# Optimization experiments

Hardware: AMD Instinct MI355X
Metric: run time of the kernel (lower is better)

Reference implementation:

```python
import jax, jax.numpy as jnp
import numpy as np
from jax import lax

B, T, C = 2, 2048, 2048
H, KV = 16, 4
D = C // H          # 128 head_dim
EPS = 1e-5
THETA = 10000.0
NEG = -1e9


def setup_inputs() -> dict:
    key = jax.random.key(0)
    ks = jax.random.split(key, 12)
    x = jax.random.normal(ks[0], (B, T, C), dtype=jnp.float32)
    s_in = 1.0 / np.sqrt(C)
    s_attn = 1.0 / np.sqrt(C)
    Wq = jax.random.normal(ks[1], (C, H * D), jnp.float32) * s_in
    Wk = jax.random.normal(ks[2], (C, KV * D), jnp.float32) * s_in
    Wv = jax.random.normal(ks[3], (C, KV * D), jnp.float32) * s_in
    Wo = jax.random.normal(ks[4], (H * D, C), jnp.float32) * s_attn
    bq = jnp.zeros((H * D,), jnp.float32)
    bk = jnp.zeros((KV * D,), jnp.float32)
    bv = jnp.zeros((KV * D,), jnp.float32)
    bo = jnp.zeros((C,), jnp.float32)
    qn_w = jnp.ones((D,), jnp.float32)
    kn_w = jnp.ones((D,), jnp.float32)
    # rotary tables: freqs_cis[t, j] = exp(i * t * theta^(-2j/D))
    inv_freq = 1.0 / (THETA ** (jnp.arange(0, D, 2, dtype=jnp.float32) / D))  # [D/2]
    angles = jnp.arange(T, dtype=jnp.float32)[:, None] * inv_freq[None, :]    # [T, D/2]
    freqs_cos = jnp.cos(angles)
    freqs_sin = jnp.sin(angles)
    # additive causal mask [1,1,T,T]
    causal = jnp.tril(jnp.ones((T, T), dtype=bool))
    mask = jnp.where(causal, 0.0, NEG).astype(jnp.float32)[None, None]
    return {"x": x, "Wq": Wq, "bq": bq, "Wk": Wk, "bk": bk, "Wv": Wv, "bv": bv,
            "Wo": Wo, "bo": bo, "qn_w": qn_w, "kn_w": kn_w,
            "freqs_cos": freqs_cos, "freqs_sin": freqs_sin, "mask": mask}


def _rmsnorm(h, w):
    var = jnp.mean(jnp.square(h), axis=-1, keepdims=True)
    return h * jax.lax.rsqrt(var + EPS) * w


def _rope(h, cos, sin):
    # h: [B,T,n,D]; cos/sin: [T, D/2] -> broadcast [1,T,1,D/2]
    hr = h.reshape(*h.shape[:-1], D // 2, 2)
    a, b = hr[..., 0], hr[..., 1]
    c = cos[None, :, None, :]
    s = sin[None, :, None, :]
    out = jnp.stack([a * c - b * s, a * s + b * c], axis=-1)
    return out.reshape(h.shape)


def reference(x, Wq, bq, Wk, bk, Wv, bv, Wo, bo, qn_w, kn_w, freqs_cos, freqs_sin, mask):
    q = (x @ Wq + bq).reshape(B, T, H, D)
    k = (x @ Wk + bk).reshape(B, T, KV, D)
    v = (x @ Wv + bv).reshape(B, T, KV, D)
    q = _rmsnorm(q, qn_w)
    k = _rmsnorm(k, kn_w)
    q = _rope(q, freqs_cos, freqs_sin)
    k = _rope(k, freqs_cos, freqs_sin)
    # GQA: repeat kv heads (interleaved, matching jnp.repeat on axis=2)
    k = jnp.repeat(k, H // KV, axis=2)
    v = jnp.repeat(v, H // KV, axis=2)
    q, k, v = (jnp.swapaxes(t, 1, 2) for t in (q, k, v))  # [B,H,T,D]
    scale = 1.0 / jnp.sqrt(jnp.float32(D))
    scores = jnp.einsum('bhid,bhjd->bhij', q, k) * scale + mask
    scores = scores - lax.stop_gradient(jnp.max(scores, axis=-1, keepdims=True))
    w = jnp.exp(scores)
    w = w / jnp.sum(w, axis=-1, keepdims=True)
    out = jnp.einsum('bhij,bhjd->bhid', w, v)
    out = jnp.swapaxes(out, 1, 2).reshape(B, T, H * D)
    return out @ Wo + bo
```

## Files before the change

kernel.cpp:

```cpp
#include <hip/hip_runtime.h>

typedef __bf16 bf16_t;
typedef __bf16 bf16x8 __attribute__((ext_vector_type(8)));
typedef __bf16 bf16x4 __attribute__((ext_vector_type(4)));
typedef float f32x4 __attribute__((ext_vector_type(4)));
typedef unsigned int u32;

#define B_    2
#define T_    2048
#define C_    2048
#define H_    16
#define KV_   4
#define D_    128
#define NT_   4096
#define NQKV_ 3072

__device__ __forceinline__ void gload16(const void* g, void* l) {
  __builtin_amdgcn_global_load_lds((const __attribute__((address_space(1))) u32*)g,
                                   (__attribute__((address_space(3))) u32*)l, 16, 0, 0);
}

__global__ __launch_bounds__(256) void k_convert(const float* __restrict__ x,
                                                 bf16_t* __restrict__ y, int n4) {
  int i = blockIdx.x * 256 + threadIdx.x;
  if (i >= n4) return;
  float4 v = ((const float4*)x)[i];
  bf16x4 o;
  o[0] = (bf16_t)v.x; o[1] = (bf16_t)v.y; o[2] = (bf16_t)v.z; o[3] = (bf16_t)v.w;
  ((bf16x4*)y)[i] = o;
}

__global__ __launch_bounds__(256) void k_transpose(const float* __restrict__ W,
                                                   bf16_t* __restrict__ Wt, int K, int N) {
  __shared__ float tile[32][33];
  int n0 = blockIdx.x * 32, k0 = blockIdx.y * 32;
  int tx = threadIdx.x & 31, ty = threadIdx.x >> 5;
#pragma unroll
  for (int r = 0; r < 32; r += 8)
    tile[ty + r][tx] = W[(size_t)(k0 + ty + r) * N + n0 + tx];
  __syncthreads();
#pragma unroll
  for (int r = 0; r < 32; r += 8)
    Wt[(size_t)(n0 + ty + r) * K + k0 + tx] = (bf16_t)tile[tx][ty + r];
}

__global__ void k_bias(const float* __restrict__ bq, const float* __restrict__ bk,
                       const float* __restrict__ bv, float* __restrict__ o) {
  int i = blockIdx.x * 256 + threadIdx.x;
  if (i < 2048) o[i] = bq[i];
  else if (i < 2560) o[i] = bk[i - 2048];
  else if (i < 3072) o[i] = bv[i - 2560];
}

__global__ __launch_bounds__(256) void k_gemm(const bf16_t* __restrict__ A,
                                              const bf16_t* __restrict__ Wt,
                                              const float* __restrict__ bias,
                                              float* __restrict__ Cout, int NTOT) {
  constexpr int K = 2048;
  __shared__ __align__(16) bf16_t As[2][128 * 32];
  __shared__ __align__(16) bf16_t Bs[2][128 * 32];
  const int tid = threadIdx.x;
  const int lane = tid & 63, w = tid >> 6;
  const int c = lane & 15, g = lane >> 4;
  const int wr = w >> 1, wc = w & 1;
  const int m0 = blockIdx.y * 128, n0 = blockIdx.x * 128;
  const int wb = w * 64;

  const f32x4 fz = {0.f, 0.f, 0.f, 0.f};
  f32x4 acc[4][4];
#pragma unroll
  for (int m = 0; m < 4; ++m)
#pragma unroll
    for (int n = 0; n < 4; ++n) acc[m][n] = fz;

  auto stage = [&](int kt, int buf) {
    const int k0 = kt * 32;
#pragma unroll
    for (int i = 0; i < 2; ++i) {
      int lu = i * 256 + wb;
      int lp = lu + lane;
      gload16(A  + (size_t)(m0 + (lp >> 2)) * K + k0 + (lp & 3) * 8, As[buf] + lu * 8);
      gload16(Wt + (size_t)(n0 + (lp >> 2)) * K + k0 + (lp & 3) * 8, Bs[buf] + lu * 8);
    }
  };

  stage(0, 0);
  int cur = 0;
  for (int kt = 0; kt < K / 32; ++kt) {
    __syncthreads();
    if (kt + 1 < K / 32) stage(kt + 1, cur ^ 1);
    bf16x8 a[4], bb[4];
#pragma unroll
    for (int m = 0; m < 4; ++m)
      a[m] = *(const bf16x8*)(As[cur] + (wr * 64 + m * 16 + c) * 32 + g * 8);
#pragma unroll
    for (int n = 0; n < 4; ++n)
      bb[n] = *(const bf16x8*)(Bs[cur] + (wc * 64 + n * 16 + c) * 32 + g * 8);
#pragma unroll
    for (int m = 0; m < 4; ++m)
#pragma unroll
      for (int n = 0; n < 4; ++n)
        acc[m][n] = __builtin_amdgcn_mfma_f32_16x16x32_bf16(a[m], bb[n], acc[m][n], 0, 0, 0);
    cur ^= 1;
  }

#pragma unroll
  for (int n = 0; n < 4; ++n) {
    const int col = n0 + wc * 64 + n * 16 + c;
    const float bn = bias[col];
#pragma unroll
    for (int m = 0; m < 4; ++m) {
      const int row = m0 + wr * 64 + m * 16 + g * 4;
#pragma unroll
      for (int r = 0; r < 4; ++r)
        Cout[(size_t)(row + r) * NTOT + col] = acc[m][n][r] + bn;
    }
  }
}

__global__ __launch_bounds__(256) void k_rmsrope(const float* __restrict__ qkv,
                                                 const float* __restrict__ qw,
                                                 const float* __restrict__ kw,
                                                 const float* __restrict__ fc,
                                                 const float* __restrict__ fs,
                                                 bf16_t* __restrict__ Qb,
                                                 bf16_t* __restrict__ Kb,
                                                 bf16_t* __restrict__ Vt) {
  const int bt = blockIdx.x;
  const int u = blockIdx.y * 4 + (threadIdx.x >> 6);
  const int lane = threadIdx.x & 63;
  const int b = bt >> 11, t = bt & (T_ - 1);
  int off;
  if (u < 16) off = u * 128;
  else if (u < 20) off = 2048 + (u - 16) * 128;
  else off = 2560 + (u - 20) * 128;
  const float2 ab = *(const float2*)(qkv + (size_t)bt * NQKV_ + off + 2 * lane);
  const float a = ab.x, bv_ = ab.y;
  if (u < 20) {
    float ssq = a * a + bv_ * bv_;
#pragma unroll
    for (int o = 32; o; o >>= 1) ssq += __shfl_xor(ssq, o, 64);
    const float r = rsqrtf(ssq * (1.0f / 128.0f) + 1e-5f);
    const float* wgt = (u < 16) ? qw : kw;
    const float a2 = a * r * wgt[2 * lane];
    const float b2 = bv_ * r * wgt[2 * lane + 1];
    const float cs = fc[t * 64 + lane], sn = fs[t * 64 + lane];
    const float o0 = a2 * cs - b2 * sn;
    const float o1 = a2 * sn + b2 * cs;
    const u32 pk = ((u32)__builtin_bit_cast(unsigned short, (bf16_t)o1) << 16) |
                   (u32)__builtin_bit_cast(unsigned short, (bf16_t)o0);
    if (u < 16)
      *(u32*)(Qb + ((size_t)(b * H_ + u) * T_ + t) * D_ + 2 * lane) = pk;
    else
      *(u32*)(Kb + ((size_t)(b * KV_ + (u - 16)) * T_ + t) * D_ + 2 * lane) = pk;
  } else {
    const int kv = u - 20;
    bf16_t* vp = Vt + (size_t)(b * KV_ + kv) * D_ * T_;
    vp[(size_t)(2 * lane) * T_ + t] = (bf16_t)a;
    vp[(size_t)(2 * lane + 1) * T_ + t] = (bf16_t)bv_;
  }
}

__global__ __launch_bounds__(256) void k_attn(const bf16_t* __restrict__ Q,
                                              const bf16_t* __restrict__ K,
                                              const bf16_t* __restrict__ Vt,
                                              bf16_t* __restrict__ Aout) {
  const int pi = blockIdx.x, h = blockIdx.y, b = blockIdx.z;
  const int tid = threadIdx.x, w = tid >> 6, lane = tid & 63;
  const int c = lane & 15, g = lane >> 4;
  const int kv = h >> 2;

  __shared__ __align__(16) bf16_t Ks[2][64 * 128];
  __shared__ __align__(16) bf16_t Vs[2][128 * 64];
  __shared__ __align__(16) bf16_t P[4][16][72];

  const bf16_t* Kp = K + (size_t)(b * KV_ + kv) * T_ * D_;
  const bf16_t* Vp = Vt + (size_t)(b * KV_ + kv) * D_ * T_;
  const float scale = 0.08838834764831845f;
  const f32x4 fz = {0.f, 0.f, 0.f, 0.f};

  int krow[4], kcol[4], vrow[4], vcol[4];
#pragma unroll
  for (int i = 0; i < 4; ++i) {
    const int ck = i * 256 + w * 64 + lane;
    krow[i] = ck >> 4;
    kcol[i] = (((ck & 15) ^ ((ck >> 4) & 7)) * 8);
    vrow[i] = ck >> 3;
    vcol[i] = (((ck & 7) ^ ((ck >> 3) & 7)) * 8);
  }

  auto stage = [&](int k0, int buf) {
#pragma unroll
    for (int i = 0; i < 4; ++i) {
      const int lu = (i * 256 + w * 64) * 8;
      gload16(Kp + (size_t)(k0 + krow[i]) * D_ + kcol[i], Ks[buf] + lu);
      gload16(Vp + (size_t)vrow[i] * T_ + k0 + vcol[i], Vs[buf] + lu);
    }
  };

#pragma unroll 1
  for (int ph = 0; ph < 2; ++ph) {
    const int qt = (ph == 0) ? pi : 31 - pi;
    const int q0 = qt * 64;
    const int nkt = qt + 1;

    const bf16_t* Qp = Q + ((size_t)(b * H_ + h) * T_ + q0 + w * 16 + c) * D_;
    bf16x8 qf[4];
#pragma unroll
    for (int ks = 0; ks < 4; ++ks) qf[ks] = *(const bf16x8*)(Qp + ks * 32 + g * 8);

    f32x4 o[8];
#pragma unroll
    for (int d = 0; d < 8; ++d) o[d] = fz;
    float mr[4], lr[4];
#pragma unroll
    for (int r = 0; r < 4; ++r) { mr[r] = -__builtin_inff(); lr[r] = 0.f; }

    if (ph == 1) __syncthreads();
    stage(0, 0);
    int cur = 0;

#pragma unroll 1
    for (int kt = 0; kt < nkt; ++kt) {
      __syncthreads();
      if (kt + 1 < nkt) stage((kt + 1) * 64, cur ^ 1);
      const int k0 = kt * 64;
      const char* Kc = (const char*)(Ks[cur]);
      const char* Vc = (const char*)(Vs[cur]);
      const int sw = (c & 7) << 4;

      f32x4 s[4];
#pragma unroll
      for (int jf = 0; jf < 4; ++jf) {
        f32x4 sj = fz;
#pragma unroll
        for (int ks = 0; ks < 4; ++ks) {
          bf16x8 kf = *(const bf16x8*)(Kc + (jf * 16 + c) * 256 + (((ks * 4 + g) * 16) ^ sw));
          sj = __builtin_amdgcn_mfma_f32_16x16x32_bf16(qf[ks], kf, sj, 0, 0, 0);
        }
        s[jf] = sj;
      }
      if (kt == qt) {
#pragma unroll
        for (int jf = 0; jf < 4; ++jf) {
          const int key = k0 + jf * 16 + c;
#pragma unroll
          for (int r = 0; r < 4; ++r) {
            const int qr = q0 + w * 16 + g * 4 + r;
            s[jf][r] = (key <= qr) ? s[jf][r] * scale : -1e30f;
          }
        }
      } else {
#pragma unroll
        for (int jf = 0; jf < 4; ++jf)
#pragma unroll
          for (int r = 0; r < 4; ++r) s[jf][r] *= scale;
      }
      float tm[4];
#pragma unroll
      for (int r = 0; r < 4; ++r) {
        tm[r] = fmaxf(fmaxf(s[0][r], s[1][r]), fmaxf(s[2][r], s[3][r]));
        tm[r] = fmaxf(tm[r], __shfl_xor(tm[r], 1, 64));
        tm[r] = fmaxf(tm[r], __shfl_xor(tm[r], 2, 64));
        tm[r] = fmaxf(tm[r], __shfl_xor(tm[r], 4, 64));
        tm[r] = fmaxf(tm[r], __shfl_xor(tm[r], 8, 64));
      }
      float al[4], rs[4];
#pragma unroll
      for (int r = 0; r < 4; ++r) {
        const float nm = fmaxf(mr[r], tm[r]);
        al[r] = __expf(mr[r] - nm);
        mr[r] = nm;
        rs[r] = 0.f;
      }
#pragma unroll
      for (int jf = 0; jf < 4; ++jf)
#pragma unroll
        for (int r = 0; r < 4; ++r) {
          const float p = __expf(s[jf][r] - mr[r]);
          s[jf][r] = p;
          rs[r] += p;
        }
#pragma unroll
      for (int r = 0; r < 4; ++r) {
        rs[r] += __shfl_xor(rs[r], 1, 64);
        rs[r] += __shfl_xor(rs[r], 2, 64);
        rs[r] += __shfl_xor(rs[r], 4, 64);
        rs[r] += __shfl_xor(rs[r], 8, 64);
        lr[r] = lr[r] * al[r] + rs[r];
      }
#pragma unroll
      for (int d = 0; d < 8; ++d)
#pragma unroll
        for (int r = 0; r < 4; ++r) o[d][r] *= al[r];
#pragma unroll
      for (int jf = 0; jf < 4; ++jf)
#pragma unroll
        for (int r = 0; r < 4; ++r)
          P[w][g * 4 + r][jf * 16 + c] = (bf16_t)s[jf][r];
#pragma unroll
      for (int ks2 = 0; ks2 < 2; ++ks2) {
        const bf16x8 pa = *(const bf16x8*)&P[w][c][ks2 * 32 + g * 8];
#pragma unroll
        for (int d = 0; d < 8; ++d) {
          const bf16x8 vf = *(const bf16x8*)(Vc + (d * 16 + c) * 128 + (((ks2 * 4 + g) * 16) ^ sw));
          o[d] = __builtin_amdgcn_mfma_f32_16x16x32_bf16(pa, vf, o[d], 0, 0, 0);
        }
      }
      cur ^= 1;
    }

    float inv[4];
#pragma unroll
    for (int r = 0; r < 4; ++r) inv[r] = 1.0f / lr[r];
#pragma unroll
    for (int d = 0; d < 8; ++d)
#pragma unroll
      for (int r = 0; r < 4; ++r)
        Aout[(size_t)(b * T_ + q0 + w * 16 + g * 4 + r) * C_ + h * D_ + d * 16 + c] =
            (bf16_t)(o[d][r] * inv[r]);
  }
}

extern "C" void kernel_launch(void* const* d_in, const int* in_sizes, int n_in,
                              void* d_out, int out_size, void* d_ws, size_t ws_size,
                              hipStream_t stream) {
  const float* x  = (const float*)d_in[0];
  const float* Wq = (const float*)d_in[1];
  const float* bq = (const float*)d_in[2];
  const float* Wk = (const float*)d_in[3];
  const float* bk = (const float*)d_in[4];
  const float* Wv = (const float*)d_in[5];
  const float* bv = (const float*)d_in[6];
  const float* Wo = (const float*)d_in[7];
  const float* bo = (const float*)d_in[8];
  const float* qw = (const float*)d_in[9];
  const float* kw = (const float*)d_in[10];
  const float* fc = (const float*)d_in[11];
  const float* fs = (const float*)d_in[12];
  float* out = (float*)d_out;

  char* p = (char*)d_ws;
  bf16_t* xb   = (bf16_t*)p; p += (size_t)NT_ * C_ * 2;
  bf16_t* Wqkv = (bf16_t*)p; p += (size_t)NQKV_ * C_ * 2;
  bf16_t* Wot  = (bf16_t*)p; p += (size_t)C_ * C_ * 2;
  float*  qkv  = (float*)p;  p += (size_t)NT_ * NQKV_ * 4;
  bf16_t* Qb   = (bf16_t*)p; p += (size_t)B_ * H_ * T_ * D_ * 2;
  bf16_t* Kb   = (bf16_t*)p; p += (size_t)B_ * KV_ * T_ * D_ * 2;
  bf16_t* Vt   = (bf16_t*)p; p += (size_t)B_ * KV_ * T_ * D_ * 2;
  float*  bqkv = (float*)p;  p += NQKV_ * 4;
  bf16_t* attn = xb;

  k_convert<<<NT_ * C_ / 4 / 256, 256, 0, stream>>>(x, xb, NT_ * C_ / 4);
  k_transpose<<<dim3(64, 64), 256, 0, stream>>>(Wq, Wqkv, 2048, 2048);
  k_transpose<<<dim3(16, 64), 256, 0, stream>>>(Wk, Wqkv + (size_t)2048 * 2048, 2048, 512);
  k_transpose<<<dim3(16, 64), 256, 0, stream>>>(Wv, Wqkv + (size_t)2560 * 2048, 2048, 512);
  k_transpose<<<dim3(64, 64), 256, 0, stream>>>(Wo, Wot, 2048, 2048);
  k_bias<<<12, 256, 0, stream>>>(bq, bk, bv, bqkv);
  k_gemm<<<dim3(NQKV_ / 128, NT_ / 128), 256, 0, stream>>>(xb, Wqkv, bqkv, qkv, NQKV_);
  k_rmsrope<<<dim3(NT_, 6), 256, 0, stream>>>(qkv, qw, kw, fc, fs, Qb, Kb, Vt);
  k_attn<<<dim3(16, H_, B_), 256, 0, stream>>>(Qb, Kb, Vt, attn);
  k_gemm<<<dim3(C_ / 128, NT_ / 128), 256, 0, stream>>>(attn, Wot, bo, out, C_);
}
```

Baseline: 429.9 us.

## Restructure GEMM into 256x128 tiles with triple-buffered swizzled LDS pipeline

```diff
diff --git a/kernel.cpp b/kernel.cpp
--- a/kernel.cpp
+++ b/kernel.cpp
@@ -52,19 +52,35 @@
   else if (i < 3072) o[i] = bv[i - 2560];
 }
 
-__global__ __launch_bounds__(256) void k_gemm(const bf16_t* __restrict__ A,
-                                              const bf16_t* __restrict__ Wt,
-                                              const float* __restrict__ bias,
-                                              float* __restrict__ Cout, int NTOT) {
+__global__ __launch_bounds__(512, 2) void k_gemm(const bf16_t* __restrict__ A,
+                                                 const bf16_t* __restrict__ Wt,
+                                                 const float* __restrict__ bias,
+                                                 float* __restrict__ Cout, int NTOT) {
   constexpr int K = 2048;
-  __shared__ __align__(16) bf16_t As[2][128 * 32];
-  __shared__ __align__(16) bf16_t Bs[2][128 * 32];
+  constexpr int NK = K / 64;
+  __shared__ __align__(16) bf16_t Asr[3][256 * 64];
+  __shared__ __align__(16) bf16_t Bsr[3][128 * 64];
   const int tid = threadIdx.x;
   const int lane = tid & 63, w = tid >> 6;
   const int c = lane & 15, g = lane >> 4;
   const int wr = w >> 1, wc = w & 1;
-  const int m0 = blockIdx.y * 128, n0 = blockIdx.x * 128;
-  const int wb = w * 64;
+  const int m0 = blockIdx.y * 256, n0 = blockIdx.x * 128;
+
+  int arow[4], asc[4], brow[2], bsc[2];
+#pragma unroll
+  for (int i = 0; i < 4; ++i) {
+    const int ck = i * 512 + w * 64 + lane;
+    arow[i] = ck >> 3; asc[i] = ((ck & 7) ^ ((ck >> 3) & 7)) * 8;
+  }
+#pragma unroll
+  for (int j = 0; j < 2; ++j) {
+    const int ck = j * 512 + w * 64 + lane;
+    brow[j] = ck >> 3; bsc[j] = ((ck & 7) ^ ((ck >> 3) & 7)) * 8;
+  }
+  const int swz0 = ((0 * 4 + g) ^ (c & 7)) * 8;
+  const int swz1 = ((1 * 4 + g) ^ (c & 7)) * 8;
+  const int aro = (wr * 64 + c) * 64;
+  const int bro = (wc * 64 + c) * 64;
 
   const f32x4 fz = {0.f, 0.f, 0.f, 0.f};
   f32x4 acc[4][4];
@@ -73,35 +89,81 @@
 #pragma unroll
     for (int n = 0; n < 4; ++n) acc[m][n] = fz;
 
-  auto stage = [&](int kt, int buf) {
-    const int k0 = kt * 32;
-#pragma unroll
-    for (int i = 0; i < 2; ++i) {
-      int lu = i * 256 + wb;
-      int lp = lu + lane;
-      gload16(A  + (size_t)(m0 + (lp >> 2)) * K + k0 + (lp & 3) * 8, As[buf] + lu * 8);
-      gload16(Wt + (size_t)(n0 + (lp >> 2)) * K + k0 + (lp & 3) * 8, Bs[buf] + lu * 8);
-    }
+  auto stageA2 = [&](int ts, int sl, int i0) {
+    const int k0 = ts * 64;
+#pragma unroll
+    for (int i = i0; i < i0 + 2; ++i)
+      gload16(A + (size_t)(m0 + arow[i]) * K + k0 + asc[i],
+              Asr[sl] + (i * 512 + w * 64) * 8);
   };
-
-  stage(0, 0);
-  int cur = 0;
-  for (int kt = 0; kt < K / 32; ++kt) {
-    __syncthreads();
-    if (kt + 1 < K / 32) stage(kt + 1, cur ^ 1);
-    bf16x8 a[4], bb[4];
+  auto stageB1 = [&](int ts, int sl, int j) {
+    const int k0 = ts * 64;
+    gload16(Wt + (size_t)(n0 + brow[j]) * K + k0 + bsc[j],
+            Bsr[sl] + (j * 512 + w * 64) * 8);
+  };
+
+  stageA2(0, 0, 0); stageA2(0, 0, 2); stageB1(0, 0, 0); stageB1(0, 0, 1);
+  stageA2(1, 1, 0); stageA2(1, 1, 2); stageB1(1, 1, 0); stageB1(1, 1, 1);
+  asm volatile("s_waitcnt vmcnt(6)" ::: "memory");
+  __builtin_amdgcn_s_barrier();
+
+  int slot = 0;
+#pragma unroll 1
+  for (int t = 0; t < NK; ++t) {
+    const int sl2 = (slot >= 1) ? slot - 1 : 2;
+    const int ts = (t + 2 < NK) ? t + 2 : NK - 1;
+    const bf16_t* Ap = Asr[slot];
+    const bf16_t* Bp = Bsr[slot];
+
+    bf16x8 af[4][2], b01[2][2];
+#pragma unroll
+    for (int m = 0; m < 4; ++m) {
+      af[m][0] = *(const bf16x8*)(Ap + aro + m * 1024 + swz0);
+      af[m][1] = *(const bf16x8*)(Ap + aro + m * 1024 + swz1);
+    }
+#pragma unroll
+    for (int n = 0; n < 2; ++n) {
+      b01[n][0] = *(const bf16x8*)(Bp + bro + n * 1024 + swz0);
+      b01[n][1] = *(const bf16x8*)(Bp + bro + n * 1024 + swz1);
+    }
+    stageA2(ts, sl2, 0); stageB1(ts, sl2, 0);
+    __builtin_amdgcn_s_barrier();
+    asm volatile("s_waitcnt lgkmcnt(0)" ::: "memory");
+    __builtin_amdgcn_sched_barrier(0);
+    __builtin_amdgcn_s_setprio(1);
 #pragma unroll
     for (int m = 0; m < 4; ++m)
-      a[m] = *(const bf16x8*)(As[cur] + (wr * 64 + m * 16 + c) * 32 + g * 8);
-#pragma unroll
-    for (int n = 0; n < 4; ++n)
-      bb[n] = *(const bf16x8*)(Bs[cur] + (wc * 64 + n * 16 + c) * 32 + g * 8);
+#pragma unroll
+      for (int n = 0; n < 2; ++n) {
+        acc[m][n] = __builtin_amdgcn_mfma_f32_16x16x32_bf16(af[m][0], b01[n][0], acc[m][n], 0, 0, 0);
+        acc[m][n] = __builtin_amdgcn_mfma_f32_16x16x32_bf16(af[m][1], b01[n][1], acc[m][n], 0, 0, 0);
+      }
+    __builtin_amdgcn_s_setprio(0);
+    __builtin_amdgcn_s_barrier();
+
+    bf16x8 b23[2][2];
+#pragma unroll
+    for (int n = 0; n < 2; ++n) {
+      b23[n][0] = *(const bf16x8*)(Bp + bro + (n + 2) * 1024 + swz0);
+      b23[n][1] = *(const bf16x8*)(Bp + bro + (n + 2) * 1024 + swz1);
+    }
+    stageA2(ts, sl2, 2); stageB1(ts, sl2, 1);
+    __builtin_amdgcn_s_barrier();
+    asm volatile("s_waitcnt lgkmcnt(0)" ::: "memory");
+    __builtin_amdgcn_sched_barrier(0);
+    __builtin_amdgcn_s_setprio(1);
 #pragma unroll
     for (int m = 0; m < 4; ++m)
 #pragma unroll
-      for (int n = 0; n < 4; ++n)
-        acc[m][n] = __builtin_amdgcn_mfma_f32_16x16x32_bf16(a[m], bb[n], acc[m][n], 0, 0, 0);
-    cur ^= 1;
+      for (int n = 0; n < 2; ++n) {
+        acc[m][n + 2] = __builtin_amdgcn_mfma_f32_16x16x32_bf16(af[m][0], b23[n][0], acc[m][n + 2], 0, 0, 0);
+        acc[m][n + 2] = __builtin_amdgcn_mfma_f32_16x16x32_bf16(af[m][1], b23[n][1], acc[m][n + 2], 0, 0, 0);
+      }
+    __builtin_amdgcn_s_setprio(0);
+    asm volatile("s_waitcnt vmcnt(6)" ::: "memory");
+    __builtin_amdgcn_s_barrier();
+    __builtin_amdgcn_sched_barrier(0);
+    slot = (slot == 2) ? 0 : slot + 1;
   }
 
 #pragma unroll
@@ -357,8 +419,8 @@
   k_transpose<<<dim3(16, 64), 256, 0, stream>>>(Wv, Wqkv + (size_t)2560 * 2048, 2048, 512);
   k_transpose<<<dim3(64, 64), 256, 0, stream>>>(Wo, Wot, 2048, 2048);
   k_bias<<<12, 256, 0, stream>>>(bq, bk, bv, bqkv);
-  k_gemm<<<dim3(NQKV_ / 128, NT_ / 128), 256, 0, stream>>>(xb, Wqkv, bqkv, qkv, NQKV_);
+  k_gemm<<<dim3(NQKV_ / 128, NT_ / 256), 512, 0, stream>>>(xb, Wqkv, bqkv, qkv, NQKV_);
   k_rmsrope<<<dim3(NT_, 6), 256, 0, stream>>>(qkv, qw, kw, fc, fs, Qb, Kb, Vt);
   k_attn<<<dim3(16, H_, B_), 256, 0, stream>>>(Qb, Kb, Vt, attn);
-  k_gemm<<<dim3(C_ / 128, NT_ / 128), 256, 0, stream>>>(attn, Wot, bo, out, C_);
-}
+  k_gemm<<<dim3(C_ / 128, NT_ / 256), 512, 0, stream>>>(attn, Wot, bo, out, C_);
+}
```

Measured after the change: 384.9 us. 1.12x faster.
